# Optimization experiments

Hardware: AMD Instinct MI355X
Metric: run time of the kernel (lower is better)

The kernel has to match this reference:

```python
import jax, jax.numpy as jnp
import numpy as np

ARCH = (1024, 2048, 2048, 512)
STEPS = 20
LR = 0.1
BATCH = 4096


def setup_inputs() -> dict:
    key = jax.random.key(0)
    ks = jax.random.split(key, 1 + len(ARCH) - 1)
    x = jax.random.normal(ks[0], (BATCH, ARCH[0]), dtype=jnp.float32)
    inp = {"x": x}
    # forward layers: weight (out, in) as in torch nn.Linear, orthogonal-ish init gain sqrt(2)
    for i in range(len(ARCH) - 1):
        fan_in = ARCH[i]
        W = jax.random.normal(ks[1 + i], (ARCH[i + 1], fan_in), dtype=jnp.float32) * jnp.sqrt(2.0 / fan_in)
        inp[f"W{i}"] = W
        inp[f"b{i}"] = jnp.zeros((ARCH[i + 1],), dtype=jnp.float32)
    return inp


def _errors(r, Ws):
    # errors[-1] = r[-1]; errors[i] = r[i] - tanh(F.linear(r[i+1], W_i.T)) = r[i] - tanh(r[i+1] @ W_i)
    errs = [None] * len(ARCH)
    errs[-1] = r[-1]
    for i in range(len(Ws) - 1, -1, -1):
        errs[i] = r[i] - jnp.tanh(r[i + 1] @ Ws[i])  # (B, arch[i])
    return errs


def _pc_forward(x, Ws, bs):
    # initialize states with a no-grad feedforward pass (torch.no_grad -> stop_gradient)
    r = [x]
    t = x
    for W, b in zip(Ws, bs):
        t = jnp.tanh(t @ W.T + b)
        r.append(jax.lax.stop_gradient(t))

    def step(carry, _):
        r = list(carry)
        errs = _errors(r, Ws)
        new_r = [r[0]]  # r[0] = x, fixed
        for i in range(1, len(ARCH)):
            feedback = errs[i - 1] @ Ws[i - 1].T  # F.linear(errors[i-1], W)
            new_r.append(r[i] + LR * (-errs[i] + feedback))
        return tuple(new_r), None

    r, _ = jax.lax.scan(step, tuple(r), None, length=STEPS)
    r = list(r)
    final_errs = _errors(r, Ws)
    total_error = 0.5 * sum(jnp.sum(e * e) for e in final_errs)
    return r[-1], total_error


def reference(x, W0, b0, W1, b1, W2, b2):
    Ws = [W0, W1, W2]
    bs = [b0, b1, b2]
    return _pc_forward(x, Ws, bs)
```

## Files before the change

kernel.cpp:

```cpp
#include <hip/hip_runtime.h>

typedef unsigned short u16;
typedef __bf16 bf16_t;
typedef bf16_t bf16x8 __attribute__((ext_vector_type(8)));
typedef u16 u16x8 __attribute__((ext_vector_type(8)));
typedef float f32x4 __attribute__((ext_vector_type(4)));

__device__ __forceinline__ u16 f2bf(float f) {
    unsigned u = __builtin_bit_cast(unsigned, f);
    u += 0x7fffu + ((u >> 16) & 1u);
    return (u16)(u >> 16);
}
__device__ __forceinline__ float bf2f(u16 h) {
    unsigned u = ((unsigned)h) << 16;
    return __builtin_bit_cast(float, u);
}
__device__ __forceinline__ float fast_tanh(float x) {
    x = fminf(fmaxf(x, -20.f), 20.f);
    float e = __expf(2.f * x);
    return (e - 1.f) * __builtin_amdgcn_rcpf(e + 1.f);
}

__device__ __forceinline__ void gload_lds16(const void* g, void* l) {
    __builtin_amdgcn_global_load_lds((__attribute__((address_space(1))) void*)(g),
                                     (__attribute__((address_space(3))) void*)(l),
                                     16, 0, 0);
}

__device__ __forceinline__ size_t boff(int m, int n, int N) {
    return (size_t)((m >> 7) * (N >> 5) + (n >> 5)) * 4096
         + (size_t)((((n >> 3) & 3) << 10) + ((m & 127) << 3) + (n & 7));
}


__global__ void cvt_bf16(const float* __restrict__ src, u16* __restrict__ dst, int n4) {
    int i = blockIdx.x * blockDim.x + threadIdx.x;
    if (i < n4) {
        float4 v = ((const float4*)src)[i];
        ushort4 o;
        o.x = f2bf(v.x); o.y = f2bf(v.y); o.z = f2bf(v.z); o.w = f2bf(v.w);
        ((ushort4*)dst)[i] = o;
    }
}

__global__ void transpose_cvt(const float* __restrict__ W, u16* __restrict__ WT, int R, int C) {
    __shared__ float tile[32][33];
    int c0 = blockIdx.x * 32, r0 = blockIdx.y * 32;
    int tx = threadIdx.x & 31, ty = threadIdx.x >> 5;
#pragma unroll
    for (int i = 0; i < 32; i += 8)
        tile[ty + i][tx] = W[(size_t)(r0 + ty + i) * C + (c0 + tx)];
    __syncthreads();
#pragma unroll
    for (int i = 0; i < 32; i += 8)
        WT[(size_t)(c0 + ty + i) * R + (r0 + tx)] = f2bf(tile[tx][ty + i]);
}

__global__ void blockify(const u16* __restrict__ src, u16* __restrict__ dst, int K) {
    const int nk = K >> 5;
    const int rb = blockIdx.x / nk, cb = blockIdx.x % nk;
    const int t = threadIdx.x;
    const int kloc = (t & 7) * 4;
    u16* d = dst + (size_t)blockIdx.x * 4096 + ((kloc >> 3) << 10) + (kloc & 7);
    const u16* s = src + (size_t)(rb * 128) * K + cb * 32 + kloc;
#pragma unroll
    for (int p = 0; p < 4; ++p) {
        int row = (t >> 3) + p * 32;
        *(ushort4*)(d + row * 8) = *(const ushort4*)(s + (size_t)row * K);
    }
}


struct Seg {
    const u16* A; const u16* B;
    const float* rsrc; const float* bias;
    const u16* esub;
    float* outf; u16* outbf;
    int K, N, blkStart, mode, accum;
};
struct Phase {
    Seg seg[3];
    int bEnd0, bEnd1;
};

__global__ __launch_bounds__(256, 4) void pc_phase(Phase ph, float* __restrict__ errAcc) {
    __shared__ u16 As[4096];
    __shared__ u16 Bs[4096];
    __shared__ float red[4];

    const int bid = blockIdx.x;
    const int segi = (bid >= ph.bEnd0 ? 1 : 0) + (bid >= ph.bEnd1 ? 1 : 0);

    const int local = bid - ph.seg[segi].blkStart;
    const int bx = local >> 5;
    const int by = local & 31;
    const int K = ph.seg[segi].K;

    const int tid  = threadIdx.x;
    const int wave = tid >> 6, lane = tid & 63;
    const int q    = lane >> 4, ln = lane & 15;
    const int wrow = (wave >> 1) * 64, wcol = (wave & 1) * 64;

    const int nk = K >> 5;
    const u16* tA = ph.seg[segi].A + (size_t)by * nk * 4096 + wave * 1024 + lane * 8;
    const u16* tB = ph.seg[segi].B + (size_t)bx * nk * 4096 + wave * 1024 + lane * 8;
    u16* lA0 = &As[wave * 1024];
    u16* lA1 = &As[wave * 1024 + 512];
    u16* lB0 = &Bs[wave * 1024];
    u16* lB1 = &Bs[wave * 1024 + 512];

    f32x4 acc[4][4];
#pragma unroll
    for (int i = 0; i < 4; ++i)
#pragma unroll
        for (int j = 0; j < 4; ++j)
            acc[i][j] = (f32x4){0.f, 0.f, 0.f, 0.f};

    const u16* asrd = &As[q * 1024 + (wrow + ln) * 8];
    const u16* bsrd = &Bs[q * 1024 + (wcol + ln) * 8];

    for (int k = 0; k < nk; ++k) {
        const size_t kb = (size_t)k * 4096;
        gload_lds16(tA + kb, lA0);
        gload_lds16(tA + kb + 512, lA1);
        gload_lds16(tB + kb, lB0);
        gload_lds16(tB + kb + 512, lB1);
        __syncthreads();

        bf16x8 a[4], b[4];
#pragma unroll
        for (int mt = 0; mt < 4; ++mt)
            a[mt] = __builtin_bit_cast(bf16x8, *(const u16x8*)&asrd[mt * 128]);
#pragma unroll
        for (int nt = 0; nt < 4; ++nt)
            b[nt] = __builtin_bit_cast(bf16x8, *(const u16x8*)&bsrd[nt * 128]);
#pragma unroll
        for (int mt = 0; mt < 4; ++mt)
#pragma unroll
            for (int nt = 0; nt < 4; ++nt)
                acc[mt][nt] = __builtin_amdgcn_mfma_f32_16x16x32_bf16(
                    a[mt], b[nt], acc[mt][nt], 0, 0, 0);
        __syncthreads();
    }

    const int N = ph.seg[segi].N;
    const int mode = ph.seg[segi].mode;
    const int accum = ph.seg[segi].accum;
    const float* rsrc = ph.seg[segi].rsrc;
    const float* bias = ph.seg[segi].bias;
    const u16* esub = ph.seg[segi].esub;
    float* outf = ph.seg[segi].outf;
    u16* outbf = ph.seg[segi].outbf;

    const int rowA0 = by * 128;
    const int rowB0 = bx * 128;

    float lsum = 0.f;
    const int ncol0 = rowB0 + wcol + ln;
#pragma unroll
    for (int mt = 0; mt < 4; ++mt) {
#pragma unroll
        for (int r = 0; r < 4; ++r) {
            int m = rowA0 + wrow + mt * 16 + q * 4 + r;
            size_t offm = (size_t)m * N;
#pragma unroll
            for (int nt = 0; nt < 4; ++nt) {
                int n = ncol0 + nt * 16;
                size_t idx = offm + n;
                size_t bidx = boff(m, n, N);
                float c = acc[mt][nt][r];
                if (mode == 0) {
                    float v = fast_tanh(c + bias[n]);
                    outf[idx] = v; outbf[bidx] = f2bf(v);
                } else if (mode == 1) {
                    float v = rsrc[idx] - fast_tanh(c);
                    outbf[bidx] = f2bf(v);
                    if (accum) lsum += v * v;
                } else if (mode == 2) {
                    float v = rsrc[idx] + 0.1f * (c - bf2f(esub[bidx]));
                    outf[idx] = v; outbf[bidx] = f2bf(v);
                } else {
                    float v = 0.9f * rsrc[idx] + 0.1f * c;
                    outf[idx] = v; outbf[bidx] = f2bf(v);
                    if (accum) lsum += v * v;
                }
            }
        }
    }

    if (accum) {
        lsum *= 0.5f;
#pragma unroll
        for (int o = 32; o > 0; o >>= 1) lsum += __shfl_down(lsum, o);
        if (lane == 0) red[wave] = lsum;
        __syncthreads();
        if (tid == 0) atomicAdd(errAcc, red[0] + red[1] + red[2] + red[3]);
    }
}


extern "C" void kernel_launch(void* const* d_in, const int* in_sizes, int n_in,
                              void* d_out, int out_size, void* d_ws, size_t ws_size,
                              hipStream_t stream) {
    const float* x  = (const float*)d_in[0];
    const float* W0 = (const float*)d_in[1];
    const float* b0 = (const float*)d_in[2];
    const float* W1 = (const float*)d_in[3];
    const float* b1 = (const float*)d_in[4];
    const float* W2 = (const float*)d_in[5];
    const float* b2 = (const float*)d_in[6];

    const int Bz = 4096;

    char* ws = (char*)d_ws;
    size_t off = 0;
    auto alloc = [&](size_t bytes) -> char* {
        char* p = ws + off;
        off += (bytes + 255) & ~(size_t)255;
        return p;
    };

    float* r1f = (float*)alloc((size_t)Bz * 2048 * 4);
    float* r2f = (float*)alloc((size_t)Bz * 2048 * 4);
    u16*   r1b = (u16*)  alloc((size_t)Bz * 2048 * 2);
    u16*   r2b = (u16*)  alloc((size_t)Bz * 2048 * 2);
    u16*   r3b = (u16*)  alloc((size_t)Bz * 512 * 2);
    u16*   e0b = (u16*)  alloc((size_t)Bz * 1024 * 2);
    u16*   e1b = (u16*)  alloc((size_t)Bz * 2048 * 2);
    u16*   e2b = (u16*)  alloc((size_t)Bz * 2048 * 2);
    u16*   xb  = (u16*)  alloc((size_t)Bz * 1024 * 2);
    u16*   W0b = (u16*)  alloc((size_t)2048 * 1024 * 2);
    u16*   W0t = (u16*)  alloc((size_t)1024 * 2048 * 2);
    u16*   W1b = (u16*)  alloc((size_t)2048 * 2048 * 2);
    u16*   W1t = (u16*)  alloc((size_t)2048 * 2048 * 2);
    u16*   W2b = (u16*)  alloc((size_t)512 * 2048 * 2);
    u16*   W2t = (u16*)  alloc((size_t)2048 * 512 * 2);
    u16*   tmp = (u16*)  alloc((size_t)2048 * 2048 * 2);

    float* r3f    = (float*)d_out;
    float* errAcc = ((float*)d_out) + (size_t)Bz * 512;

    auto blkify = [&](const u16* s, u16* d, int M, int K) {
        blockify<<<(M / 128) * (K / 32), 256, 0, stream>>>(s, d, K);
    };

    cvt_bf16<<<(Bz * 1024 / 4) / 256, 256, 0, stream>>>(x, tmp, Bz * 1024 / 4);
    blkify(tmp, xb, Bz, 1024);
    cvt_bf16<<<(2048 * 1024 / 4) / 256, 256, 0, stream>>>(W0, tmp, 2048 * 1024 / 4);
    blkify(tmp, W0b, 2048, 1024);
    cvt_bf16<<<(2048 * 2048 / 4) / 256, 256, 0, stream>>>(W1, tmp, 2048 * 2048 / 4);
    blkify(tmp, W1b, 2048, 2048);
    cvt_bf16<<<(512 * 2048 / 4) / 256, 256, 0, stream>>>(W2, tmp, 512 * 2048 / 4);
    blkify(tmp, W2b, 512, 2048);
    transpose_cvt<<<dim3(1024 / 32, 2048 / 32), 256, 0, stream>>>(W0, tmp, 2048, 1024);
    blkify(tmp, W0t, 1024, 2048);
    transpose_cvt<<<dim3(2048 / 32, 2048 / 32), 256, 0, stream>>>(W1, tmp, 2048, 2048);
    blkify(tmp, W1t, 2048, 2048);
    transpose_cvt<<<dim3(2048 / 32, 512 / 32),  256, 0, stream>>>(W2, tmp, 512, 2048);
    blkify(tmp, W2t, 2048, 512);

    hipMemsetAsync(errAcc, 0, 4, stream);

    auto mkseg = [&](const u16* A, const u16* B, int K, int N,
                     const float* rsrc, const float* bias, const u16* esub,
                     float* outf, u16* outbf, int mode, int accum, int blkStart) {
        Seg s;
        s.A = A; s.B = B; s.rsrc = rsrc; s.bias = bias; s.esub = esub;
        s.outf = outf; s.outbf = outbf;
        s.K = K; s.N = N; s.blkStart = blkStart;
        s.mode = mode; s.accum = accum;
        return s;
    };
    auto nblk = [&](int N) { return (N / 128) * (Bz / 128); };

    auto launch1 = [&](Seg s0) {
        Phase ph;
        int b0 = nblk(s0.N);
        ph.seg[0] = s0; ph.seg[1] = s0; ph.seg[2] = s0;
        ph.bEnd0 = b0; ph.bEnd1 = b0;
        pc_phase<<<b0, 256, 0, stream>>>(ph, errAcc);
    };
    auto launch3 = [&](Seg s0, Seg s1, Seg s2) {
        Phase ph;
        int b0 = nblk(s0.N), b1 = nblk(s1.N), b2 = nblk(s2.N);
        s1.blkStart = b0; s2.blkStart = b0 + b1;
        ph.seg[0] = s0; ph.seg[1] = s1; ph.seg[2] = s2;
        ph.bEnd0 = b0; ph.bEnd1 = b0 + b1;
        pc_phase<<<b0 + b1 + b2, 256, 0, stream>>>(ph, errAcc);
    };

    launch1(mkseg(xb,  W0b, 1024, 2048, nullptr, b0, nullptr, r1f, r1b, 0, 0, 0));
    launch1(mkseg(r1b, W1b, 2048, 2048, nullptr, b1, nullptr, r2f, r2b, 0, 0, 0));
    launch1(mkseg(r2b, W2b, 2048, 512,  nullptr, b2, nullptr, r3f, r3b, 0, 0, 0));

    for (int s = 0; s < 20; ++s) {
        int last = (s == 19) ? 1 : 0;
        launch3(mkseg(r2b, W1t, 2048, 2048, r1f, nullptr, nullptr, nullptr, e1b, 1, 0, 0),
                mkseg(r1b, W0t, 2048, 1024, x,   nullptr, nullptr, nullptr, e0b, 1, 0, 0),
                mkseg(r3b, W2t, 512,  2048, r2f, nullptr, nullptr, nullptr, e2b, 1, 0, 0));
        launch3(mkseg(e1b, W1b, 2048, 2048, r2f, nullptr, e2b, r2f, r2b, 2, 0, 0),
                mkseg(e2b, W2b, 2048, 512,  r3f, nullptr, nullptr, r3f, r3b, 3, last, 0),
                mkseg(e0b, W0b, 1024, 2048, r1f, nullptr, e1b, r1f, r1b, 2, 0, 0));
    }

    launch3(mkseg(r2b, W1t, 2048, 2048, r1f, nullptr, nullptr, nullptr, e1b, 1, 1, 0),
            mkseg(r1b, W0t, 2048, 1024, x,   nullptr, nullptr, nullptr, e0b, 1, 1, 0),
            mkseg(r3b, W2t, 512,  2048, r2f, nullptr, nullptr, nullptr, e2b, 1, 1, 0));
}
```

Before: 4.106 ms.

## Drop fp32 hidden states and stage blocked bf16 epilogue through LDS

Removes the fp32 copies of hidden states r1 and r2 and keeps only the blocked bf16 versions, reading the residual source as bf16 instead of fp32. The epilogue now stages tiles through shared memory in four quarter passes, so global reads of rsrc/esub and writes of the bf16 output become coalesced 16-byte accesses in the blocked layout instead of scattered 2-byte ones. This aims to cut epilogue memory traffic, at the cost of extra barriers and precision loss, since the state updates now accumulate in bf16 over 20 steps.

```diff
diff --git a/kernel.cpp b/kernel.cpp
--- a/kernel.cpp
+++ b/kernel.cpp
@@ -27,10 +27,6 @@
                                      16, 0, 0);
 }
 
-__device__ __forceinline__ size_t boff(int m, int n, int N) {
-    return (size_t)((m >> 7) * (N >> 5) + (n >> 5)) * 4096
-         + (size_t)((((n >> 3) & 3) << 10) + ((m & 127) << 3) + (n & 7));
-}
 
 
 __global__ void cvt_bf16(const float* __restrict__ src, u16* __restrict__ dst, int n4) {
@@ -73,9 +69,12 @@
 
 struct Seg {
     const u16* A; const u16* B;
-    const float* rsrc; const float* bias;
+    const u16* rsrcb;
+    const float* rsrcf;
+    const float* bias;
     const u16* esub;
-    float* outf; u16* outbf;
+    float* outf;
+    u16* outbf;
     int K, N, blkStart, mode, accum;
 };
 struct Phase {
@@ -146,7 +145,8 @@
     const int N = ph.seg[segi].N;
     const int mode = ph.seg[segi].mode;
     const int accum = ph.seg[segi].accum;
-    const float* rsrc = ph.seg[segi].rsrc;
+    const u16* rsrcb = ph.seg[segi].rsrcb;
+    const float* rsrcf = ph.seg[segi].rsrcf;
     const float* bias = ph.seg[segi].bias;
     const u16* esub = ph.seg[segi].esub;
     float* outf = ph.seg[segi].outf;
@@ -154,38 +154,69 @@
 
     const int rowA0 = by * 128;
     const int rowB0 = bx * 128;
+    const size_t regionOff = ((size_t)by * (N >> 5) + bx * 4) * 4096;
+    const u16* rsrcR = rsrcb ? rsrcb + regionOff : nullptr;
+    const u16* esubR = esub ? esub + regionOff : nullptr;
+    u16* outR = outbf + regionOff;
+
+    const int o0 = tid * 16;
+    const int ch = o0 >> 8;
+    const size_t gq = (size_t)(ch >> 2) * 4096 + (size_t)(ch & 3) * 1024 + (o0 & 255);
 
     float lsum = 0.f;
-    const int ncol0 = rowB0 + wcol + ln;
-#pragma unroll
-    for (int mt = 0; mt < 4; ++mt) {
-#pragma unroll
-        for (int r = 0; r < 4; ++r) {
-            int m = rowA0 + wrow + mt * 16 + q * 4 + r;
-            size_t offm = (size_t)m * N;
-#pragma unroll
-            for (int nt = 0; nt < 4; ++nt) {
-                int n = ncol0 + nt * 16;
-                size_t idx = offm + n;
-                size_t bidx = boff(m, n, N);
-                float c = acc[mt][nt][r];
-                if (mode == 0) {
-                    float v = fast_tanh(c + bias[n]);
-                    outf[idx] = v; outbf[bidx] = f2bf(v);
-                } else if (mode == 1) {
-                    float v = rsrc[idx] - fast_tanh(c);
-                    outbf[bidx] = f2bf(v);
-                    if (accum) lsum += v * v;
-                } else if (mode == 2) {
-                    float v = rsrc[idx] + 0.1f * (c - bf2f(esub[bidx]));
-                    outf[idx] = v; outbf[bidx] = f2bf(v);
-                } else {
-                    float v = 0.9f * rsrc[idx] + 0.1f * c;
-                    outf[idx] = v; outbf[bidx] = f2bf(v);
-                    if (accum) lsum += v * v;
+    const int myHalf = wave >> 1;
+
+#pragma unroll
+    for (int qq = 0; qq < 4; ++qq) {
+        const size_t g = gq + qq * 256;
+        if (mode == 1 || mode == 2) {
+            *(u16x8*)(As + o0)     = *(const u16x8*)(rsrcR + g);
+            *(u16x8*)(As + o0 + 8) = *(const u16x8*)(rsrcR + g + 8);
+        }
+        if (mode == 2) {
+            *(u16x8*)(Bs + o0)     = *(const u16x8*)(esubR + g);
+            *(u16x8*)(Bs + o0 + 8) = *(const u16x8*)(esubR + g + 8);
+        }
+        __syncthreads();
+
+        if ((qq >> 1) == myHalf) {
+            const int mtlo = (qq & 1) * 2;
+#pragma unroll
+            for (int mi = 0; mi < 2; ++mi) {
+                const int mt = mtlo + mi;
+#pragma unroll
+                for (int r = 0; r < 4; ++r) {
+                    const int rl = mi * 16 + q * 4 + r;
+                    const int m = rowA0 + wrow + mt * 16 + q * 4 + r;
+#pragma unroll
+                    for (int nt = 0; nt < 4; ++nt) {
+                        const int nrel = wcol + nt * 16 + ln;
+                        const int o = (nrel >> 3) * 256 + rl * 8 + (nrel & 7);
+                        const float c = acc[mt][nt][r];
+                        float v;
+                        if (mode == 0) {
+                            v = fast_tanh(c + bias[rowB0 + nrel]);
+                            if (outf) outf[(size_t)m * N + rowB0 + nrel] = v;
+                        } else if (mode == 1) {
+                            v = bf2f(As[o]) - fast_tanh(c);
+                            if (accum) lsum += v * v;
+                        } else if (mode == 2) {
+                            v = bf2f(As[o]) + 0.1f * (c - bf2f(Bs[o]));
+                        } else {
+                            const size_t idx = (size_t)m * N + rowB0 + nrel;
+                            v = 0.9f * rsrcf[idx] + 0.1f * c;
+                            outf[idx] = v;
+                            if (accum) lsum += v * v;
+                        }
+                        As[o] = f2bf(v);
+                    }
                 }
             }
         }
+        __syncthreads();
+        *(u16x8*)(outR + g)     = *(const u16x8*)(As + o0);
+        *(u16x8*)(outR + g + 8) = *(const u16x8*)(As + o0 + 8);
+        __syncthreads();
     }
 
     if (accum) {
@@ -220,8 +251,6 @@
         return p;
     };
 
-    float* r1f = (float*)alloc((size_t)Bz * 2048 * 4);
-    float* r2f = (float*)alloc((size_t)Bz * 2048 * 4);
     u16*   r1b = (u16*)  alloc((size_t)Bz * 2048 * 2);
     u16*   r2b = (u16*)  alloc((size_t)Bz * 2048 * 2);
     u16*   r3b = (u16*)  alloc((size_t)Bz * 512 * 2);
@@ -262,13 +291,13 @@
     hipMemsetAsync(errAcc, 0, 4, stream);
 
     auto mkseg = [&](const u16* A, const u16* B, int K, int N,
-                     const float* rsrc, const float* bias, const u16* esub,
-                     float* outf, u16* outbf, int mode, int accum, int blkStart) {
+                     const u16* rsrcb, const float* rsrcf, const float* bias,
+                     const u16* esub, float* outf, u16* outbf,
+                     int mode, int accum) {
         Seg s;
-        s.A = A; s.B = B; s.rsrc = rsrc; s.bias = bias; s.esub = esub;
-        s.outf = outf; s.outbf = outbf;
-        s.K = K; s.N = N; s.blkStart = blkStart;
-        s.mode = mode; s.accum = accum;
+        s.A = A; s.B = B; s.rsrcb = rsrcb; s.rsrcf = rsrcf; s.bias = bias;
+        s.esub = esub; s.outf = outf; s.outbf = outbf;
+        s.K = K; s.N = N; s.blkStart = 0; s.mode = mode; s.accum = accum;
         return s;
     };
     auto nblk = [&](int N) { return (N / 128) * (Bz / 128); };
@@ -289,21 +318,21 @@
         pc_phase<<<b0 + b1 + b2, 256, 0, stream>>>(ph, errAcc);
     };
 
-    launch1(mkseg(xb,  W0b, 1024, 2048, nullptr, b0, nullptr, r1f, r1b, 0, 0, 0));
-    launch1(mkseg(r1b, W1b, 2048, 2048, nullptr, b1, nullptr, r2f, r2b, 0, 0, 0));
-    launch1(mkseg(r2b, W2b, 2048, 512,  nullptr, b2, nullptr, r3f, r3b, 0, 0, 0));
+    launch1(mkseg(xb,  W0b, 1024, 2048, nullptr, nullptr, b0, nullptr, nullptr, r1b, 0, 0));
+    launch1(mkseg(r1b, W1b, 2048, 2048, nullptr, nullptr, b1, nullptr, nullptr, r2b, 0, 0));
+    launch1(mkseg(r2b, W2b, 2048, 512,  nullptr, nullptr, b2, nullptr, r3f,     r3b, 0, 0));
 
     for (int s = 0; s < 20; ++s) {
         int last = (s == 19) ? 1 : 0;
-        launch3(mkseg(r2b, W1t, 2048, 2048, r1f, nullptr, nullptr, nullptr, e1b, 1, 0, 0),
-                mkseg(r1b, W0t, 2048, 1024, x,   nullptr, nullptr, nullptr, e0b, 1, 0, 0),
-                mkseg(r3b, W2t, 512,  2048, r2f, nullptr, nullptr, nullptr, e2b, 1, 0, 0));
-        launch3(mkseg(e1b, W1b, 2048, 2048, r2f, nullptr, e2b, r2f, r2b, 2, 0, 0),
-                mkseg(e2b, W2b, 2048, 512,  r3f, nullptr, nullptr, r3f, r3b, 3, last, 0),
-                mkseg(e0b, W0b, 1024, 2048, r1f, nullptr, e1b, r1f, r1b, 2, 0, 0));
-    }
-
-    launch3(mkseg(r2b, W1t, 2048, 2048, r1f, nullptr, nullptr, nullptr, e1b, 1, 1, 0),
-            mkseg(r1b, W0t, 2048, 1024, x,   nullptr, nullptr, nullptr, e0b, 1, 1, 0),
-            mkseg(r3b, W2t, 512,  2048, r2f, nullptr, nullptr, nullptr, e2b, 1, 1, 0));
-}
+        launch3(mkseg(r2b, W1t, 2048, 2048, r1b, nullptr, nullptr, nullptr, nullptr, e1b, 1, 0),
+                mkseg(r1b, W0t, 2048, 1024, xb,  nullptr, nullptr, nullptr, nullptr, e0b, 1, 0),
+                mkseg(r3b, W2t, 512,  2048, r2b, nullptr, nullptr, nullptr, nullptr, e2b, 1, 0));
+        launch3(mkseg(e1b, W1b, 2048, 2048, r2b, nullptr, nullptr, e2b, nullptr, r2b, 2, 0),
+                mkseg(e2b, W2b, 2048, 512,  nullptr, r3f, nullptr, nullptr, r3f,  r3b, 3, last),
+                mkseg(e0b, W0b, 1024, 2048, r1b, nullptr, nullptr, e1b, nullptr, r1b, 2, 0));
+    }
+
+    launch3(mkseg(r2b, W1t, 2048, 2048, r1b, nullptr, nullptr, nullptr, nullptr, e1b, 1, 1),
+            mkseg(r1b, W0t, 2048, 1024, xb,  nullptr, nullptr, nullptr, nullptr, e0b, 1, 1),
+            mkseg(r3b, W2t, 512,  2048, r2b, nullptr, nullptr, nullptr, nullptr, e2b, 1, 1));
+}
```

After: 4.097 ms. About the same (-0.2%).
